# Kernel optimization log

Hardware: AMD Instinct MI355X
Metric: run time of the kernel (lower is better)

The kernel has to match this reference:

```python
import jax, jax.numpy as jnp
import numpy as np

B, N, D, HID, NB, NC = 64, 256, 1024, 512, 2, 1000
EPS = 1e-5

def _ln(x, g, b):
    m = x.mean(-1, keepdims=True)
    v = ((x - m) ** 2).mean(-1, keepdims=True)
    return (x - m) / jnp.sqrt(v + EPS) * g + b

def _gelu(x):
    return jax.nn.gelu(x, approximate=False)

def _knn_adjacency(x, k):
    # x: [N, D] -> symmetric-normalized kNN adjacency with self loops, [N, N]
    n = x.shape[0]
    sq = jnp.sum(x * x, axis=-1)
    d2 = sq[:, None] + sq[None, :] - 2.0 * (x @ x.T)
    d2 = jnp.where(jnp.eye(n, dtype=bool), jnp.inf, d2)  # exclude self from kNN
    idx = jax.lax.top_k(-d2, k)[1]                       # [N, k] nearest neighbors
    A = jnp.zeros((n, n), x.dtype).at[jnp.arange(n)[:, None], idx].set(1.0)
    A = jnp.maximum(A, A.T) + jnp.eye(n, dtype=x.dtype)  # symmetrize + self loops
    dinv = jax.lax.rsqrt(A.sum(-1))                      # D^{-1/2}
    return A * dinv[:, None] * dinv[None, :]

def setup_inputs() -> dict:
    key = jax.random.key(0)
    ks = jax.random.split(key, 8)
    s = lambda i, shape: jax.random.normal(ks[i], shape, jnp.float32) * 0.02
    return {
        "tokens": jax.random.normal(ks[0], (B, N, D), jnp.float32),
        "W1": s(1, (NB, D, HID)), "b1": jnp.zeros((NB, HID), jnp.float32),
        "W2": s(2, (NB, HID, D)), "b2": jnp.zeros((NB, D), jnp.float32),
        "g1": jnp.ones((NB, D), jnp.float32), "be1": jnp.zeros((NB, D), jnp.float32),
        "g2": jnp.ones((NB, D), jnp.float32), "be2": jnp.zeros((NB, D), jnp.float32),
        "gr": jnp.ones((D,), jnp.float32), "br": jnp.zeros((D,), jnp.float32),
        "Wc": s(3, (D, NC)), "bc": jnp.zeros((NC,), jnp.float32),
        "k": 8,
    }

def reference(tokens, W1, b1, W2, b2, g1, be1, g2, be2, gr, br, Wc, bc, k):
    # tokens: [B, N, D] backbone features flattened to nodes (eval mode: dropout = identity)
    A = jax.vmap(lambda t: _knn_adjacency(t, k))(tokens)  # [B, N, N]
    x = tokens
    for i in range(NB):  # GraphBlock
        h = _ln(x, g1[i], be1[i])
        h = _gelu(jnp.einsum("bij,bjh->bih", A, h @ W1[i] + b1[i]))  # A_hat @ lin1
        h = jnp.einsum("bij,bjd->bid", A, h @ W2[i] + b2[i])          # A_hat @ lin2
        x = x + h
        x = x + _gelu(_ln(x, g2[i], be2[i]))
    x = _gelu(_ln(x, gr, br))      # readout
    out = x.mean(axis=1)           # graph mean-pool, [B, D]
    return out @ Wc + bc           # logits [B, NC]
```

## Files before the change

### kernel.cpp

```cpp
#include <hip/hip_runtime.h>
#include <hip/hip_bf16.h>
#include <math.h>

constexpr int Bb  = 64;
constexpr int Nn_ = 256;
constexpr int Dd  = 1024;
constexpr int Hh  = 512;
constexpr int NC  = 1000;
constexpr float LN_EPS = 1e-5f;

#define DEV __device__ __forceinline__

typedef unsigned short u16;
typedef __attribute__((ext_vector_type(8))) short bf16x8;
typedef __attribute__((ext_vector_type(4))) float f32x4;
typedef __attribute__((ext_vector_type(4))) unsigned short u16x4;

DEV float erf_fast(float x) {
    const float ax = fabsf(x);
    const float t = __builtin_amdgcn_rcpf(fmaf(0.3275911f, ax, 1.0f));
    const float y = t * (0.254829592f + t * (-0.284496736f + t * (1.421413741f +
                    t * (-1.453152027f + t * 1.061405429f))));
    const float r = 1.0f - y * __expf(-ax * ax);
    return copysignf(r, x);
}
DEV float gelu_f(float x) { return 0.5f * x * (1.0f + erf_fast(x * 0.70710678118654752f)); }
DEV u16 bfb(float x) { __hip_bfloat16 h = __float2bfloat16(x); u16 u; __builtin_memcpy(&u, &h, 2); return u; }
DEV float fromb(u16 u) { unsigned int w = (unsigned int)u << 16; float f; __builtin_memcpy(&f, &w, 4); return f; }

DEV void gload16(const void* g, void* l) {
    __builtin_amdgcn_global_load_lds(
        (const __attribute__((address_space(1))) void*)(uintptr_t)g,
        (__attribute__((address_space(3))) void*)(uintptr_t)l, 16, 0, 0);
}

enum { EP_BIAS_BF_CT = 0, EP_GELU_BF_CT = 1, EP_BF = 2, EP_SBIAS_BF = 3 };

template<int EPI>
__global__ __launch_bounds__(512) void mgemm_k(
    const u16* __restrict__ Ag, const u16* __restrict__ Bg, void* __restrict__ Cg,
    const float* __restrict__ bias, const float* __restrict__ rsA,
    int M, int Nc, int K, long sA, long sB, long sC,
    int lognx, int logny, int lognz)
{
    __shared__ __align__(16) u16 sm[2][2][128 * 32];
    const int tid = threadIdx.x;
    const int l = tid & 63, w = tid >> 6;
    const int wm = w >> 2, wn = w & 3;

    const int lid = blockIdx.x;
    const int xcd = lid & 7, idx = lid >> 3;
    int bxi, byi, z;
    if (lognz == 0) {
        bxi = idx & ((1 << lognx) - 1);
        byi = (xcd << (logny - 3)) | (idx >> lognx);
        z = 0;
    } else {
        bxi = idx & ((1 << lognx) - 1);
        byi = (idx >> lognx) & ((1 << logny) - 1);
        z = (xcd << (lognz - 3)) | (idx >> (lognx + logny));
    }
    const int bm = byi * 128, bn = bxi * 128;

    const u16* Ab  = Ag + (long)z * sA;
    const u16* Bbp = Bg + (long)z * sB;

    f32x4 acc[4][2] = {};
    const int nt = K >> 5;

    auto stage = [&](int db, int t) {
        const long kk = (long)t << 5;
        const int o = tid * 16;
        const int r = o >> 6;
        const int g = ((o >> 4) & 3) ^ ((r >> 1) & 3);
        gload16(Ab  + (long)(bm + r) * K + kk + g * 8, (char*)&sm[db][0][0] + o);
        gload16(Bbp + (long)(bn + r) * K + kk + g * 8, (char*)&sm[db][1][0] + o);
    };

    stage(0, 0);
    __syncthreads();
    for (int t = 0; t < nt; ++t) {
        const int db = t & 1;
        if (t + 1 < nt) stage(db ^ 1, t + 1);
        const int lr = l & 15, g = l >> 4;
        bf16x8 af[4], bfr[2];
        #pragma unroll
        for (int fm = 0; fm < 4; ++fm) {
            const int r = wm * 64 + fm * 16 + lr;
            af[fm] = *(const bf16x8*)((const char*)&sm[db][0][0] + r * 64 + ((g ^ ((r >> 1) & 3)) << 4));
        }
        #pragma unroll
        for (int fn = 0; fn < 2; ++fn) {
            const int r = wn * 32 + fn * 16 + lr;
            bfr[fn] = *(const bf16x8*)((const char*)&sm[db][1][0] + r * 64 + ((g ^ ((r >> 1) & 3)) << 4));
        }
        #pragma unroll
        for (int fm = 0; fm < 4; ++fm)
            #pragma unroll
            for (int fn = 0; fn < 2; ++fn)
                acc[fm][fn] = __builtin_amdgcn_mfma_f32_16x16x32_bf16(af[fm], bfr[fn], acc[fm][fn], 0, 0, 0);
        __syncthreads();
    }

    const int lr = l & 15, lg = l >> 4;
    if constexpr (EPI == EP_SBIAS_BF) {
        u16* Cb = (u16*)Cg;
        #pragma unroll
        for (int fm = 0; fm < 4; ++fm)
            #pragma unroll
            for (int fn = 0; fn < 2; ++fn) {
                const int gc = bn + wn * 32 + fn * 16 + lr;
                const float bv = bias[gc];
                #pragma unroll
                for (int rg = 0; rg < 4; ++rg) {
                    const int gm = bm + wm * 64 + fm * 16 + lg * 4 + rg;
                    Cb[(long)gm * Nc + gc] = bfb(acc[fm][fn][rg] + rsA[gm] * bv);
                }
            }
    } else if constexpr (EPI == EP_BIAS_BF_CT || EPI == EP_GELU_BF_CT) {
        #pragma unroll
        for (int fm = 0; fm < 4; ++fm) {
            const int gm0 = bm + wm * 64 + fm * 16 + lg * 4;
            #pragma unroll
            for (int fn = 0; fn < 2; ++fn) {
                const int gc = bn + wn * 32 + fn * 16 + lr;
                u16x4 vals;
                if constexpr (EPI == EP_BIAS_BF_CT) {
                    const float bv = bias[gc];
                    #pragma unroll
                    for (int rg = 0; rg < 4; ++rg) vals[rg] = bfb(acc[fm][fn][rg] + bv);
                } else {
                    #pragma unroll
                    for (int rg = 0; rg < 4; ++rg) vals[rg] = bfb(gelu_f(acc[fm][fn][rg]));
                }
                long addr;
                if constexpr (EPI == EP_BIAS_BF_CT)
                    addr = (long)(gm0 >> 8) * ((long)Nc * 256) + (long)gc * 256 + (gm0 & 255);
                else
                    addr = (long)z * sC + (long)gc * 256 + gm0;
                *(u16x4*)&((u16*)Cg)[addr] = vals;
            }
        }
    } else {
        u16* Cb = (u16*)Cg + (long)z * sC;
        #pragma unroll
        for (int fm = 0; fm < 4; ++fm)
            #pragma unroll
            for (int fn = 0; fn < 2; ++fn)
                #pragma unroll
                for (int rg = 0; rg < 4; ++rg) {
                    const int gm = bm + wm * 64 + fm * 16 + lg * 4 + rg;
                    const int gc = bn + wn * 32 + fn * 16 + lr;
                    Cb[(long)gm * Nc + gc] = bfb(acc[fm][fn][rg]);
                }
    }
}

__global__ __launch_bounds__(512) void d2mm_k(
    const u16* __restrict__ HL, const float* __restrict__ sq, float* __restrict__ d2)
{
    __shared__ __align__(16) u16 sm[2][4][128 * 32];
    const int tid = threadIdx.x;
    const int l = tid & 63, w = tid >> 6;
    const int wm = w >> 2, wn = w & 3;

    const int lid = blockIdx.x;
    const int xcd = lid & 7, q = lid >> 3;
    const int j   = q % 3;
    const int z   = (q / 3) * 8 + xcd;
    const int bm  = (j == 2) ? 128 : 0;
    const int bn  = (j == 0) ? 0 : 128;

    const u16* Hb = HL + (long)z * Nn_ * 2048;

    f32x4 acc[4][2] = {};

    auto stage = [&](int db, int t) {
        const long kk = (long)t << 5;
        const int o = tid * 16;
        const int r = o >> 6;
        const int g = ((o >> 4) & 3) ^ ((r >> 1) & 3);
        const long ka = kk + g * 8;
        gload16(Hb + (long)(bm + r) * 2048 + ka,        (char*)&sm[db][0][0] + o);
        gload16(Hb + (long)(bm + r) * 2048 + 1024 + ka, (char*)&sm[db][1][0] + o);
        gload16(Hb + (long)(bn + r) * 2048 + ka,        (char*)&sm[db][2][0] + o);
        gload16(Hb + (long)(bn + r) * 2048 + 1024 + ka, (char*)&sm[db][3][0] + o);
    };

    stage(0, 0);
    __syncthreads();
    for (int t = 0; t < 32; ++t) {
        const int db = t & 1;
        if (t + 1 < 32) stage(db ^ 1, t + 1);
        const int lr = l & 15, g = l >> 4;
        bf16x8 ah[4], al[4], bh[2], bl[2];
        #pragma unroll
        for (int fm = 0; fm < 4; ++fm) {
            const int r = wm * 64 + fm * 16 + lr;
            const int off = r * 64 + ((g ^ ((r >> 1) & 3)) << 4);
            ah[fm] = *(const bf16x8*)((const char*)&sm[db][0][0] + off);
            al[fm] = *(const bf16x8*)((const char*)&sm[db][1][0] + off);
        }
        #pragma unroll
        for (int fn = 0; fn < 2; ++fn) {
            const int r = wn * 32 + fn * 16 + lr;
            const int off = r * 64 + ((g ^ ((r >> 1) & 3)) << 4);
            bh[fn] = *(const bf16x8*)((const char*)&sm[db][2][0] + off);
            bl[fn] = *(const bf16x8*)((const char*)&sm[db][3][0] + off);
        }
        #pragma unroll
        for (int fm = 0; fm < 4; ++fm)
            #pragma unroll
            for (int fn = 0; fn < 2; ++fn) {
                acc[fm][fn] = __builtin_amdgcn_mfma_f32_16x16x32_bf16(ah[fm], bh[fn], acc[fm][fn], 0, 0, 0);
                acc[fm][fn] = __builtin_amdgcn_mfma_f32_16x16x32_bf16(ah[fm], bl[fn], acc[fm][fn], 0, 0, 0);
                acc[fm][fn] = __builtin_amdgcn_mfma_f32_16x16x32_bf16(al[fm], bh[fn], acc[fm][fn], 0, 0, 0);
            }
        __syncthreads();
    }

    const int lr = l & 15, lg = l >> 4;
    const float* sqb = sq + z * Nn_;
    float* ob = d2 + (long)z * Nn_ * Nn_;
    #pragma unroll
    for (int fm = 0; fm < 4; ++fm)
        #pragma unroll
        for (int fn = 0; fn < 2; ++fn)
            #pragma unroll
            for (int rg = 0; rg < 4; ++rg) {
                const int gm = bm + wm * 64 + fm * 16 + lg * 4 + rg;
                const int gc = bn + wn * 32 + fn * 16 + lr;
                float v = sqb[gm] + sqb[gc] - 2.0f * acc[fm][fn][rg];
                if (gm == gc) v = INFINITY;
                ob[(long)gm * Nn_ + gc] = v;
                if (j == 1) ob[(long)gc * Nn_ + gm] = v;
            }
}

__global__ __launch_bounds__(256) void clear_k(float4* __restrict__ p)
{
    p[(long)blockIdx.x * 256 + threadIdx.x] = make_float4(0.f, 0.f, 0.f, 0.f);
}

__global__ __launch_bounds__(256) void prep_k(const float* __restrict__ in, u16* __restrict__ hilo,
    float* __restrict__ sq, u16* __restrict__ lnout,
    const float* __restrict__ g, const float* __restrict__ bvec)
{
    const int w = threadIdx.x >> 6, lane = threadIdx.x & 63;
    const long row = (long)blockIdx.x * 4 + w;
    const long base = row * Dd;

    float xs[16];
    #pragma unroll
    for (int c = 0; c < 4; ++c) {
        const int idx = c * 256 + lane * 4;
        const float4 v = *(const float4*)&in[base + idx];
        xs[c*4+0] = v.x; xs[c*4+1] = v.y; xs[c*4+2] = v.z; xs[c*4+3] = v.w;
        u16x4 hi, lo;
        #pragma unroll
        for (int j = 0; j < 4; ++j) {
            hi[j] = bfb(xs[c*4+j]);
            lo[j] = bfb(xs[c*4+j] - fromb(hi[j]));
        }
        *(u16x4*)&hilo[row * 2048 + idx]        = hi;
        *(u16x4*)&hilo[row * 2048 + 1024 + idx] = lo;
    }

    float s = 0.f, s2 = 0.f;
    #pragma unroll
    for (int i = 0; i < 16; ++i) { s += xs[i]; s2 += xs[i] * xs[i]; }
    #pragma unroll
    for (int o = 32; o > 0; o >>= 1) { s += __shfl_xor(s, o); s2 += __shfl_xor(s2, o); }
    if (lane == 0) sq[row] = s2;
    const float mean = s * (1.0f / Dd);
    const float rstd = rsqrtf(s2 * (1.0f / Dd) - mean * mean + LN_EPS);

    #pragma unroll
    for (int c = 0; c < 4; ++c) {
        const int idx = c * 256 + lane * 4;
        const float4 gv = *(const float4*)&g[idx];
        const float4 bv = *(const float4*)&bvec[idx];
        const float gs[4] = {gv.x, gv.y, gv.z, gv.w};
        const float bs[4] = {bv.x, bv.y, bv.z, bv.w};
        u16x4 ov;
        #pragma unroll
        for (int j = 0; j < 4; ++j) ov[j] = bfb((xs[c*4+j] - mean) * rstd * gs[j] + bs[j]);
        *(u16x4*)&lnout[base + idx] = ov;
    }
}

__global__ __launch_bounds__(256) void transw_k(const float* __restrict__ in, u16* __restrict__ out,
                                                int R, int C, long sIn, long sOut)
{
    __shared__ u16 t[32][33];
    const int z = blockIdx.z;
    const float* ib = in + (long)z * sIn;
    u16* ob = out + (long)z * sOut;
    const int r0 = blockIdx.y * 32, c0 = blockIdx.x * 32;
    const int tr = threadIdx.x >> 3, tc4 = (threadIdx.x & 7) * 4;
    const float* p = ib + (long)(r0 + tr) * C + c0 + tc4;
    #pragma unroll
    for (int j = 0; j < 4; ++j) t[tr][tc4 + j] = bfb(p[j]);
    __syncthreads();
    u16* q = ob + (long)(c0 + tr) * R + r0 + tc4;
    #pragma unroll
    for (int j = 0; j < 4; ++j) q[j] = t[tc4 + j][tr];
}

__global__ __launch_bounds__(256) void transc_k(const float* __restrict__ Wc, float* __restrict__ WcT)
{
    __shared__ float t[32][33];
    const int r0 = blockIdx.y * 32, c0 = blockIdx.x * 32;
    const int tr = threadIdx.x >> 3, tc4 = (threadIdx.x & 7) * 4;
    #pragma unroll
    for (int j = 0; j < 4; ++j) {
        const int c = c0 + tc4 + j;
        t[tr][tc4 + j] = (c < NC) ? Wc[(long)(r0 + tr) * NC + c] : 0.f;
    }
    __syncthreads();
    const int oc = c0 + tr;
    if (oc < NC) {
        #pragma unroll
        for (int j = 0; j < 4; ++j)
            WcT[(long)oc * Dd + r0 + tc4 + j] = t[tc4 + j][tr];
    }
}

template<int LAST, int XF32>
__global__ __launch_bounds__(256) void ln2fr_k(const u16* __restrict__ hsrc,
    const void* __restrict__ xinv, u16* __restrict__ xout, u16* __restrict__ lnout,
    const float* __restrict__ g2, const float* __restrict__ be2,
    const float* __restrict__ gn, const float* __restrict__ bn)
{
    const int w = threadIdx.x >> 6, lane = threadIdx.x & 63;
    const long row = (long)blockIdx.x * 4 + w;
    const long base = row * Dd;

    float xs[16];
    #pragma unroll
    for (int c = 0; c < 4; ++c) {
        const int idx = c * 256 + lane * 4;
        const u16x4 hv = *(const u16x4*)&hsrc[base + idx];
        if constexpr (XF32) {
            const float4 xv = *(const float4*)&((const float*)xinv)[base + idx];
            xs[c*4+0] = xv.x + fromb(hv[0]);
            xs[c*4+1] = xv.y + fromb(hv[1]);
            xs[c*4+2] = xv.z + fromb(hv[2]);
            xs[c*4+3] = xv.w + fromb(hv[3]);
        } else {
            const u16x4 xv = *(const u16x4*)&((const u16*)xinv)[base + idx];
            #pragma unroll
            for (int j = 0; j < 4; ++j) xs[c*4+j] = fromb(xv[j]) + fromb(hv[j]);
        }
    }

    {
        float s = 0.f, s2 = 0.f;
        #pragma unroll
        for (int i = 0; i < 16; ++i) { s += xs[i]; s2 += xs[i] * xs[i]; }
        #pragma unroll
        for (int o = 32; o > 0; o >>= 1) { s += __shfl_xor(s, o); s2 += __shfl_xor(s2, o); }
        const float mean = s * (1.0f / Dd);
        const float rstd = rsqrtf(s2 * (1.0f / Dd) - mean * mean + LN_EPS);
        #pragma unroll
        for (int c = 0; c < 4; ++c) {
            const int idx = c * 256 + lane * 4;
            const float4 gv = *(const float4*)&g2[idx];
            const float4 bv = *(const float4*)&be2[idx];
            const float gs[4] = {gv.x, gv.y, gv.z, gv.w};
            const float bs[4] = {bv.x, bv.y, bv.z, bv.w};
            #pragma unroll
            for (int j = 0; j < 4; ++j)
                xs[c*4+j] = xs[c*4+j] + gelu_f((xs[c*4+j] - mean) * rstd * gs[j] + bs[j]);
        }
    }

    float s = 0.f, s2 = 0.f;
    #pragma unroll
    for (int i = 0; i < 16; ++i) { s += xs[i]; s2 += xs[i] * xs[i]; }
    #pragma unroll
    for (int o = 32; o > 0; o >>= 1) { s += __shfl_xor(s, o); s2 += __shfl_xor(s2, o); }
    const float mean = s * (1.0f / Dd);
    const float rstd = rsqrtf(s2 * (1.0f / Dd) - mean * mean + LN_EPS);
    #pragma unroll
    for (int c = 0; c < 4; ++c) {
        const int idx = c * 256 + lane * 4;
        const float4 gv = *(const float4*)&gn[idx];
        const float4 bv = *(const float4*)&bn[idx];
        const float gs[4] = {gv.x, gv.y, gv.z, gv.w};
        const float bs[4] = {bv.x, bv.y, bv.z, bv.w};
        u16x4 ov;
        if constexpr (LAST) {
            #pragma unroll
            for (int j = 0; j < 4; ++j) ov[j] = bfb(gelu_f((xs[c*4+j] - mean) * rstd * gs[j] + bs[j]));
        } else {
            u16x4 xo;
            #pragma unroll
            for (int j = 0; j < 4; ++j) xo[j] = bfb(xs[c*4+j]);
            *(u16x4*)&xout[base + idx] = xo;
            #pragma unroll
            for (int j = 0; j < 4; ++j) ov[j] = bfb((xs[c*4+j] - mean) * rstd * gs[j] + bs[j]);
        }
        *(u16x4*)&lnout[base + idx] = ov;
    }
}

__global__ __launch_bounds__(256) void topk_k(const float* __restrict__ d2, float* __restrict__ Aout,
                                              const int* __restrict__ kptr)
{
    const int k = *kptr;
    const int wid = threadIdx.x >> 6, lane = threadIdx.x & 63;
    const long row = (long)blockIdx.x * 4 + wid;
    const long b = row >> 8;
    const int  i = (int)(row & 255);
    const float* dr = d2 + row * Nn_;
    float v[4];
    bool sel[4] = {false, false, false, false};
    #pragma unroll
    for (int c = 0; c < 4; ++c) v[c] = dr[lane + 64 * c];
    for (int it = 0; it < k; ++it) {
        float bv = INFINITY; int bi = 1 << 20;
        #pragma unroll
        for (int c = 0; c < 4; ++c) {
            const int idx = lane + 64 * c;
            if (!sel[c] && (v[c] < bv || (v[c] == bv && idx < bi))) { bv = v[c]; bi = idx; }
        }
        #pragma unroll
        for (int o = 32; o > 0; o >>= 1) {
            float ov = __shfl_xor(bv, o); int oi = __shfl_xor(bi, o);
            if (ov < bv || (ov == bv && oi < bi)) { bv = ov; bi = oi; }
        }
        #pragma unroll
        for (int c = 0; c < 4; ++c) if (lane + 64 * c == bi) sel[c] = true;
        if (lane == 0) {
            Aout[(b * Nn_ + i) * Nn_ + bi] = 1.0f;
            Aout[(b * Nn_ + bi) * Nn_ + i] = 1.0f;
        }
    }
    if (lane == 0) Aout[(b * Nn_ + i) * Nn_ + i] = 1.0f;
}

__global__ __launch_bounds__(256) void deg_k(const float* __restrict__ A, float* __restrict__ dinv)
{
    const int wid = threadIdx.x >> 6, lane = threadIdx.x & 63;
    const long row = (long)blockIdx.x * 4 + wid;
    const float* ar = A + row * Nn_;
    float s = 0.f;
    #pragma unroll
    for (int c = 0; c < 4; ++c) s += ar[lane + 64 * c];
    #pragma unroll
    for (int o = 32; o > 0; o >>= 1) s += __shfl_down(s, o);
    if (lane == 0) dinv[row] = rsqrtf(s);
}

__global__ __launch_bounds__(256) void scalebf2_k(const float* __restrict__ A, const float* __restrict__ dinv,
                                                  u16* __restrict__ out, float* __restrict__ rsA)
{
    const int wid = threadIdx.x >> 6, lane = threadIdx.x & 63;
    const long row = (long)blockIdx.x * 4 + wid;
    const long b = row >> 8;
    const float di = dinv[row];
    const int j0 = lane * 4;
    const float4 dj = *(const float4*)&dinv[b * Nn_ + j0];
    const float4 a = *(const float4*)&A[row * Nn_ + j0];
    const float v0 = a.x * di * dj.x, v1 = a.y * di * dj.y, v2 = a.z * di * dj.z, v3 = a.w * di * dj.w;
    u16x4 o = { bfb(v0), bfb(v1), bfb(v2), bfb(v3) };
    *(u16x4*)&out[row * Nn_ + j0] = o;
    float s = v0 + v1 + v2 + v3;
    #pragma unroll
    for (int off = 32; off > 0; off >>= 1) s += __shfl_down(s, off);
    if (lane == 0) rsA[row] = s;
}

__global__ __launch_bounds__(256) void poolb_k(const u16* __restrict__ y, float* __restrict__ pooled)
{
    const int d = blockIdx.x * 256 + threadIdx.x;
    const int b = blockIdx.y;
    const u16* yb = y + (long)b * Nn_ * Dd + d;
    float s = 0.f;
    #pragma unroll 4
    for (int n = 0; n < Nn_; ++n) s += fromb(yb[(long)n * Dd]);
    pooled[b * Dd + d] = s * (1.0f / Nn_);
}

__global__ __launch_bounds__(256) void cls2_k(const float* __restrict__ pooled, const float* __restrict__ WcT,
    const float* __restrict__ bc, float* __restrict__ out)
{
    const int w = threadIdx.x >> 6, lane = threadIdx.x & 63;
    const int c = blockIdx.x * 4 + w;
    const int b = blockIdx.y;
    const float* wr = WcT + (long)c * Dd;
    const float* p  = pooled + (long)b * Dd;
    float s = 0.f;
    #pragma unroll
    for (int it = 0; it < 4; ++it) {
        const float4 wv = *(const float4*)&wr[it * 256 + lane * 4];
        const float4 pv = *(const float4*)&p[it * 256 + lane * 4];
        s += wv.x * pv.x + wv.y * pv.y + wv.z * pv.z + wv.w * pv.w;
    }
    #pragma unroll
    for (int o = 32; o > 0; o >>= 1) s += __shfl_down(s, o);
    if (lane == 0) out[(long)b * NC + c] = s + bc[c];
}

extern "C" void kernel_launch(void* const* d_in, const int* in_sizes, int n_in,
                              void* d_out, int out_size, void* d_ws, size_t ws_size,
                              hipStream_t stream)
{
    const float* tokens = (const float*)d_in[0];
    const float* W1  = (const float*)d_in[1];
    const float* b1  = (const float*)d_in[2];
    const float* W2  = (const float*)d_in[3];
    const float* b2  = (const float*)d_in[4];
    const float* g1  = (const float*)d_in[5];
    const float* be1 = (const float*)d_in[6];
    const float* g2  = (const float*)d_in[7];
    const float* be2 = (const float*)d_in[8];
    const float* gr  = (const float*)d_in[9];
    const float* br  = (const float*)d_in[10];
    const float* Wc  = (const float*)d_in[11];
    const float* bc  = (const float*)d_in[12];
    const int*   kptr = (const int*)d_in[13];

    constexpr long SZ_XD = (long)Bb * Nn_ * Dd;
    constexpr long SZ_A  = (long)Bb * Nn_ * Nn_;

    char* wp = (char*)d_ws;
    u16*   xbf    = (u16*)wp;   wp += SZ_XD * 2;
    u16*   hbuf   = (u16*)wp;   wp += SZ_XD * 2;
    u16*   bufA   = (u16*)wp;   wp += SZ_XD * 2;
    u16*   bufB   = (u16*)wp;   wp += SZ_XD * 2;
    u16*   bufC   = (u16*)wp;   wp += SZ_XD * 2;
    u16*   AmatBF = (u16*)wp;   wp += SZ_A * 2;
    u16*   W1t    = (u16*)wp;   wp += 2L * Dd * Hh * 2;
    u16*   W2t    = (u16*)wp;   wp += 2L * Hh * Dd * 2;
    float* WcT    = (float*)wp; wp += (long)NC * Dd * 4;
    float* sq     = (float*)wp; wp += (long)Bb * Nn_ * 4;
    float* dinv   = (float*)wp; wp += (long)Bb * Nn_ * 4;
    float* rsA    = (float*)wp; wp += (long)Bb * Nn_ * 4;
    float* pooled = (float*)wp; wp += (long)Bb * Dd * 4;

    u16*   hilo  = bufA;
    float* d2f   = (float*)hbuf;
    float* AmatF = (float*)xbf;
    u16*   robuf = bufA;

    const dim3 blk(256);
    const dim3 blk8(512);

    prep_k<<<Bb * Nn_ / 4, blk, 0, stream>>>(tokens, hilo, sq, bufC, g1, be1);

    d2mm_k<<<192, blk8, 0, stream>>>(hilo, sq, d2f);
    clear_k<<<(int)(SZ_A / 4 / 256), blk, 0, stream>>>((float4*)AmatF);
    topk_k<<<Bb * Nn_ / 4, blk, 0, stream>>>(d2f, AmatF, kptr);
    deg_k<<<Bb * Nn_ / 4, blk, 0, stream>>>(AmatF, dinv);
    scalebf2_k<<<Bb * Nn_ / 4, blk, 0, stream>>>(AmatF, dinv, AmatBF, rsA);

    transw_k<<<dim3(Hh / 32, Dd / 32, 2), blk, 0, stream>>>(W1, W1t, Dd, Hh, (long)Dd * Hh, (long)Hh * Dd);
    transw_k<<<dim3(Dd / 32, Hh / 32, 2), blk, 0, stream>>>(W2, W2t, Hh, Dd, (long)Hh * Dd, (long)Dd * Hh);
    transc_k<<<dim3(32, Dd / 32), blk, 0, stream>>>(Wc, WcT);

    for (int i = 0; i < 2; ++i) {
        mgemm_k<EP_BIAS_BF_CT><<<512, blk8, 0, stream>>>(
            bufC, W1t + (long)i * Hh * Dd, bufB, b1 + i * Hh, nullptr,
            Bb * Nn_, Hh, Dd, 0, 0, 0, 2, 7, 0);
        mgemm_k<EP_GELU_BF_CT><<<512, blk8, 0, stream>>>(
            AmatBF, bufB, bufA, nullptr, nullptr,
            Nn_, Hh, Nn_, (long)Nn_ * Nn_, (long)Hh * Nn_, (long)Hh * Nn_, 2, 1, 6);
        mgemm_k<EP_BF><<<512, blk8, 0, stream>>>(
            AmatBF, bufA, bufB, nullptr, nullptr,
            Nn_, Hh, Nn_, (long)Nn_ * Nn_, (long)Hh * Nn_, (long)Nn_ * Hh, 2, 1, 6);
        mgemm_k<EP_SBIAS_BF><<<1024, blk8, 0, stream>>>(
            bufB, W2t + (long)i * Dd * Hh, hbuf, b2 + i * Dd, rsA,
            Bb * Nn_, Dd, Hh, 0, 0, 0, 3, 7, 0);
        if (i == 0)
            ln2fr_k<0, 1><<<Bb * Nn_ / 4, blk, 0, stream>>>(hbuf, tokens, xbf, bufC,
                g2, be2, g1 + Dd, be1 + Dd);
        else
            ln2fr_k<1, 0><<<Bb * Nn_ / 4, blk, 0, stream>>>(hbuf, xbf, nullptr, robuf,
                g2 + Dd, be2 + Dd, gr, br);
    }

    poolb_k<<<dim3(Dd / 256, Bb), blk, 0, stream>>>(robuf, pooled);
    cls2_k<<<dim3(NC / 4, Bb), blk, 0, stream>>>(pooled, WcT, bc, (float*)d_out);
}
```

Before: 362.6 us.

## Fuse the two per-graph adjacency GEMMs into one kernel keeping GELU result in LDS

Replaces the two batched A_hat GEMM launches (A@Y with GELU, then A@Z) with a single kernel per (graph, 128-column slice). Each block keeps the A_hat rows in registers, computes GELU(A@Y) into swizzled shared memory, and reuses it for the second multiply, so the intermediate never goes to global memory. The cost is heavy register and LDS use (128KB LDS, 2 blocks/SM bound) and only 256 blocks in flight, which may reduce occupancy and parallelism.

```diff
diff --git a/kernel.cpp b/kernel.cpp
--- a/kernel.cpp
+++ b/kernel.cpp
@@ -34,7 +34,7 @@
         (__attribute__((address_space(3))) void*)(uintptr_t)l, 16, 0, 0);
 }
 
-enum { EP_BIAS_BF_CT = 0, EP_GELU_BF_CT = 1, EP_BF = 2, EP_SBIAS_BF = 3 };
+enum { EP_BIAS_BF_CT = 0, EP_SBIAS_BF = 3 };
 
 template<int EPI>
 __global__ __launch_bounds__(512) void mgemm_k(
@@ -117,43 +117,118 @@
                     Cb[(long)gm * Nc + gc] = bfb(acc[fm][fn][rg] + rsA[gm] * bv);
                 }
             }
-    } else if constexpr (EPI == EP_BIAS_BF_CT || EPI == EP_GELU_BF_CT) {
+    } else {
         #pragma unroll
         for (int fm = 0; fm < 4; ++fm) {
             const int gm0 = bm + wm * 64 + fm * 16 + lg * 4;
             #pragma unroll
             for (int fn = 0; fn < 2; ++fn) {
                 const int gc = bn + wn * 32 + fn * 16 + lr;
+                const float bv = bias[gc];
                 u16x4 vals;
-                if constexpr (EPI == EP_BIAS_BF_CT) {
-                    const float bv = bias[gc];
-                    #pragma unroll
-                    for (int rg = 0; rg < 4; ++rg) vals[rg] = bfb(acc[fm][fn][rg] + bv);
-                } else {
-                    #pragma unroll
-                    for (int rg = 0; rg < 4; ++rg) vals[rg] = bfb(gelu_f(acc[fm][fn][rg]));
-                }
-                long addr;
-                if constexpr (EPI == EP_BIAS_BF_CT)
-                    addr = (long)(gm0 >> 8) * ((long)Nc * 256) + (long)gc * 256 + (gm0 & 255);
-                else
-                    addr = (long)z * sC + (long)gc * 256 + gm0;
+                #pragma unroll
+                for (int rg = 0; rg < 4; ++rg) vals[rg] = bfb(acc[fm][fn][rg] + bv);
+                const long addr = (long)(gm0 >> 8) * ((long)Nc * 256) + (long)gc * 256 + (gm0 & 255);
                 *(u16x4*)&((u16*)Cg)[addr] = vals;
             }
         }
-    } else {
-        u16* Cb = (u16*)Cg + (long)z * sC;
+    }
+}
+
+__global__ __launch_bounds__(512, 2) void ayy_k(
+    const u16* __restrict__ Ahat, const u16* __restrict__ Y1t, u16* __restrict__ AZ)
+{
+    __shared__ __align__(16) u16 sY[128 * 256];
+    __shared__ __align__(16) u16 sZ[128 * 256];
+
+    const int tid = threadIdx.x;
+    const int l = tid & 63, w = tid >> 6;
+    const int wm = w >> 1, wn = w & 1;
+
+    const int lid = blockIdx.x;
+    const int xcd = lid & 7, idx = lid >> 3;
+    const int cs = idx & 3;
+    const int z  = xcd * 8 + (idx >> 2);
+
+    const u16* Ab = Ahat + (long)z * Nn_ * Nn_;
+    const u16* Yb = Y1t + (long)z * Hh * Nn_ + (long)(cs * 128) * Nn_;
+
+    #pragma unroll
+    for (int i = 0; i < 8; ++i) {
+        const int o = i * 8192 + tid * 16;
+        const int c = o >> 9;
+        const int wb = (o & 511) ^ ((c & 7) << 4);
+        gload16((const char*)Yb + (long)c * 512 + wb, (char*)sY + o);
+    }
+
+    const int lr = l & 15, g = l >> 4;
+    bf16x8 af[4][8];
+    #pragma unroll
+    for (int fm = 0; fm < 4; ++fm) {
+        const int r = wm * 64 + fm * 16 + lr;
+        #pragma unroll
+        for (int ks = 0; ks < 8; ++ks)
+            af[fm][ks] = *(const bf16x8*)(Ab + (long)r * Nn_ + ks * 32 + g * 8);
+    }
+
+    __syncthreads();
+
+    f32x4 acc[4][4] = {};
+    #pragma unroll
+    for (int ks = 0; ks < 8; ++ks) {
+        bf16x8 bfr[4];
+        #pragma unroll
+        for (int fn = 0; fn < 4; ++fn) {
+            const int c = wn * 64 + fn * 16 + lr;
+            const int kb = (ks * 64 + g * 16) ^ ((c & 7) << 4);
+            bfr[fn] = *(const bf16x8*)((const char*)sY + c * 512 + kb);
+        }
         #pragma unroll
         for (int fm = 0; fm < 4; ++fm)
             #pragma unroll
-            for (int fn = 0; fn < 2; ++fn)
-                #pragma unroll
-                for (int rg = 0; rg < 4; ++rg) {
-                    const int gm = bm + wm * 64 + fm * 16 + lg * 4 + rg;
-                    const int gc = bn + wn * 32 + fn * 16 + lr;
-                    Cb[(long)gm * Nc + gc] = bfb(acc[fm][fn][rg]);
-                }
-    }
+            for (int fn = 0; fn < 4; ++fn)
+                acc[fm][fn] = __builtin_amdgcn_mfma_f32_16x16x32_bf16(af[fm][ks], bfr[fn], acc[fm][fn], 0, 0, 0);
+    }
+    #pragma unroll
+    for (int fm = 0; fm < 4; ++fm)
+        #pragma unroll
+        for (int fn = 0; fn < 4; ++fn) {
+            const int c = wn * 64 + fn * 16 + lr;
+            const int r0 = wm * 64 + fm * 16 + g * 4;
+            u16x4 v;
+            #pragma unroll
+            for (int rg = 0; rg < 4; ++rg) v[rg] = bfb(gelu_f(acc[fm][fn][rg]));
+            *(u16x4*)((char*)sZ + c * 512 + ((r0 * 2) ^ ((c & 7) << 4))) = v;
+            acc[fm][fn] = f32x4{0.f, 0.f, 0.f, 0.f};
+        }
+    __syncthreads();
+
+    #pragma unroll
+    for (int ks = 0; ks < 8; ++ks) {
+        bf16x8 bfr[4];
+        #pragma unroll
+        for (int fn = 0; fn < 4; ++fn) {
+            const int c = wn * 64 + fn * 16 + lr;
+            const int kb = (ks * 64 + g * 16) ^ ((c & 7) << 4);
+            bfr[fn] = *(const bf16x8*)((const char*)sZ + c * 512 + kb);
+        }
+        #pragma unroll
+        for (int fm = 0; fm < 4; ++fm)
+            #pragma unroll
+            for (int fn = 0; fn < 4; ++fn)
+                acc[fm][fn] = __builtin_amdgcn_mfma_f32_16x16x32_bf16(af[fm][ks], bfr[fn], acc[fm][fn], 0, 0, 0);
+    }
+    u16* Ob = AZ + (long)z * Nn_ * Hh + cs * 128;
+    #pragma unroll
+    for (int fm = 0; fm < 4; ++fm)
+        #pragma unroll
+        for (int fn = 0; fn < 4; ++fn)
+            #pragma unroll
+            for (int rg = 0; rg < 4; ++rg) {
+                const int r = wm * 64 + fm * 16 + g * 4 + rg;
+                const int c = wn * 64 + fn * 16 + lr;
+                Ob[(long)r * Hh + c] = bfb(acc[fm][fn][rg]);
+            }
 }
 
 __global__ __launch_bounds__(512) void d2mm_k(
@@ -564,14 +639,9 @@
         mgemm_k<EP_BIAS_BF_CT><<<512, blk8, 0, stream>>>(
             bufC, W1t + (long)i * Hh * Dd, bufB, b1 + i * Hh, nullptr,
             Bb * Nn_, Hh, Dd, 0, 0, 0, 2, 7, 0);
-        mgemm_k<EP_GELU_BF_CT><<<512, blk8, 0, stream>>>(
-            AmatBF, bufB, bufA, nullptr, nullptr,
-            Nn_, Hh, Nn_, (long)Nn_ * Nn_, (long)Hh * Nn_, (long)Hh * Nn_, 2, 1, 6);
-        mgemm_k<EP_BF><<<512, blk8, 0, stream>>>(
-            AmatBF, bufA, bufB, nullptr, nullptr,
-            Nn_, Hh, Nn_, (long)Nn_ * Nn_, (long)Hh * Nn_, (long)Nn_ * Hh, 2, 1, 6);
+        ayy_k<<<256, blk8, 0, stream>>>(AmatBF, bufB, bufA);
         mgemm_k<EP_SBIAS_BF><<<1024, blk8, 0, stream>>>(
-            bufB, W2t + (long)i * Dd * Hh, hbuf, b2 + i * Dd, rsA,
+            bufA, W2t + (long)i * Dd * Hh, hbuf, b2 + i * Dd, rsA,
             Bb * Nn_, Dd, Hh, 0, 0, 0, 3, 7, 0);
         if (i == 0)
             ln2fr_k<0, 1><<<Bb * Nn_ / 4, blk, 0, stream>>>(hbuf, tokens, xbf, bufC,
```

After: 359.1 us. About the same (-0.9%).
